# Kernel optimization log

Measured on AMD Instinct MI355X. Metric: run time of the kernel, lower is better.

## Reference

```python
import jax, jax.numpy as jnp
import numpy as np

TAU = 0.5

def setup_inputs() -> dict:
    key = jax.random.key(0)
    kx, ky = jax.random.split(key)
    B, H = 8192, 256
    x = jax.random.normal(kx, (B, H), dtype=jnp.float32)
    y = jax.random.normal(ky, (B, H), dtype=jnp.float32)
    return {"x": x, "y": y}

def reference(x, y):
    # L2-normalize rows
    x_norm = x / jnp.linalg.norm(x, axis=1, keepdims=True)
    y_norm = y / jnp.linalg.norm(y, axis=1, keepdims=True)
    xy_norm = jnp.concatenate([x_norm, y_norm], axis=0)  # [2N, H]
    yx_norm = jnp.concatenate([y_norm, x_norm], axis=0)  # [2N, H]
    # [2N, 2N] cosine-similarity matrix (dominant memory traffic)
    sim_mat_1 = xy_norm @ xy_norm.T
    exp_mat = jnp.exp(sim_mat_1 / TAU)
    exp_row_sum = jnp.sum(exp_mat, axis=1)
    exp_diag = jnp.diagonal(exp_mat)
    denominator = exp_row_sum - exp_diag
    # diag(xy_norm @ yx_norm.T) is the row-wise dot product (avoids redundant NxN matmul)
    pos_sim = jnp.sum(xy_norm * yx_norm, axis=1)
    numerator = jnp.exp(pos_sim / TAU)
    nt_xent = -jnp.log(numerator / denominator)
    return jnp.mean(nt_xent)
```

## Files before the change

### kernel.cpp

```cpp
#include <hip/hip_runtime.h>
#include <hip/hip_bf16.h>
#include <math.h>

constexpr int NROWS = 8192;
constexpr int HDIM  = 256;
constexpr int N2    = 16384;
constexpr int TM    = 256;
constexpr int BK    = 32;
constexpr int NCHUNK = HDIM / BK;
constexpr int PIECE = TM * BK;
constexpr int NTILE = N2 / TM;
constexpr int NBLK  = NTILE * (NTILE + 1) / 2;

constexpr float PRESCALE = 1.69864357f;

typedef __attribute__((ext_vector_type(4))) float floatx4;
typedef __attribute__((ext_vector_type(8))) short shortx8;

__device__ __forceinline__ void async_copy16(const void* gptr, void* lptr) {
    __builtin_amdgcn_global_load_lds(
        (const __attribute__((address_space(1))) unsigned int*)gptr,
        (__attribute__((address_space(3))) unsigned int*)lptr, 16, 0, 0);
}

#define WAIT_VM2()   __builtin_amdgcn_s_waitcnt(0x0F72)
#define WAIT_VM0()   __builtin_amdgcn_s_waitcnt(0x0F70)
#define MEMFENCE()   __asm__ __volatile__("" ::: "memory")
#define RAW_BARRIER() do { MEMFENCE(); __builtin_amdgcn_s_barrier(); MEMFENCE(); } while (0)

#define DPP_ROW_SHL_ADD(v, CTRL) do {                                        \
    union { float f; int i; } _u, _r; _u.f = (v);                            \
    _r.i = __builtin_amdgcn_update_dpp(0, _u.i, (CTRL), 0xF, 0xF, true);     \
    (v) += _r.f; } while (0)

__global__ __launch_bounds__(256) void normalize_kernel(
    const float* __restrict__ x, const float* __restrict__ y,
    __hip_bfloat16* __restrict__ Z, float* __restrict__ pos,
    float* __restrict__ rowsum, float* __restrict__ out)
{
    const int wave = threadIdx.x >> 6, lane = threadIdx.x & 63;
    const int row  = blockIdx.x * 4 + wave;

    const float4 xv = ((const float4*)x)[row * 64 + lane];
    const float4 yv = ((const float4*)y)[row * 64 + lane];

    float sx  = xv.x*xv.x + xv.y*xv.y + xv.z*xv.z + xv.w*xv.w;
    float sy  = yv.x*yv.x + yv.y*yv.y + yv.z*yv.z + yv.w*yv.w;
    float sxy = xv.x*yv.x + xv.y*yv.y + xv.z*yv.z + xv.w*yv.w;
    #pragma unroll
    for (int m = 1; m < 64; m <<= 1) {
        sx  += __shfl_xor(sx,  m);
        sy  += __shfl_xor(sy,  m);
        sxy += __shfl_xor(sxy, m);
    }
    const float rxn = rsqrtf(sx), ryn = rsqrtf(sy);
    const float rx = rxn * PRESCALE, ry = ryn * PRESCALE;

    union { ushort4 u; __hip_bfloat16 h[4]; } zx, zy;
    zx.h[0] = __float2bfloat16(xv.x * rx); zx.h[1] = __float2bfloat16(xv.y * rx);
    zx.h[2] = __float2bfloat16(xv.z * rx); zx.h[3] = __float2bfloat16(xv.w * rx);
    zy.h[0] = __float2bfloat16(yv.x * ry); zy.h[1] = __float2bfloat16(yv.y * ry);
    zy.h[2] = __float2bfloat16(yv.z * ry); zy.h[3] = __float2bfloat16(yv.w * ry);
    ((ushort4*)Z)[row * 64 + lane]             = zx.u;
    ((ushort4*)Z)[(row + NROWS) * 64 + lane]   = zy.u;

    if (lane == 0) {
        const float p = sxy * rxn * ryn;
        pos[row]         = p;
        pos[row + NROWS] = p;
    }
    const int gt = blockIdx.x * 256 + threadIdx.x;
    if (gt < N2) rowsum[gt] = 0.f;
    if (gt == 0) out[0] = 0.f;
}

__global__ __launch_bounds__(1024, 4) void simgemm_kernel(
    const __hip_bfloat16* __restrict__ Z, float* __restrict__ rowsum)
{
    const int b = blockIdx.x;
    const int k = b & 7;
    const int m = b >> 3;
    int bi, bj;
    if (m < 36) {
        int ti = (int)((17.0f - sqrtf(289.0f - 8.0f * (float)m)) * 0.5f);
        if (m < ti * (17 - ti) / 2) ti--;
        else if (m >= (ti + 1) * (16 - ti) / 2) ti++;
        const int tj = ti + (m - ti * (17 - ti) / 2);
        bi = k * 8 + ti;
        bj = k * 8 + tj;
    } else {
        const int m2 = m - 36;
        const int hh = m2 >> 5;
        const int r  = m2 & 31;
        const int h  = hh * 8 + k;
        const int q  = h >> 1;
        const int sub = h & 1;
        int gi = 0;
        #pragma unroll
        for (int t = 6; t > 0; --t)
            if (q >= t * (15 - t) / 2) { gi = t; break; }
        const int gj = gi + 1 + (q - gi * (15 - gi) / 2);
        bi = gi * 8 + sub * 4 + (r >> 3);
        bj = gj * 8 + (r & 7);
    }
    const bool diag = (bi == bj);

    __shared__ alignas(16) __hip_bfloat16 tiles[6 * PIECE];
    __shared__ float rs[TM];
    __shared__ float cs[TM];
    __hip_bfloat16* tA = tiles;
    __hip_bfloat16* tB = tiles + PIECE;

    const int tid  = threadIdx.x;
    const int wave = tid >> 6;
    const int lane = tid & 63;
    const int wm   = wave & 3;
    const int wn   = wave >> 2;
    const int g    = lane >> 4;
    const int m15  = lane & 15;

    if (tid < TM) { rs[tid] = 0.f; cs[tid] = 0.f; }

    const int st_r0  = wave * 16 + (lane >> 2);
    const int st_c   = (lane & 3) ^ ((lane >> 3) & 3);
    const __hip_bfloat16* gA0 = Z + (size_t)(bi * TM + st_r0) * HDIM + st_c * 8;
    const __hip_bfloat16* gB0 = Z + (size_t)(bj * TM + st_r0) * HDIM + st_c * 8;
    __hip_bfloat16* lA0 = tA + (wave * 16) * BK;
    __hip_bfloat16* lB0 = tB + (wave * 16) * BK;

    const int sw = g ^ ((m15 >> 1) & 3);
    const __hip_bfloat16* rA = tA + (wm * 64 + m15) * BK + sw * 8;
    const __hip_bfloat16* rB = tB + (wn * 64 + m15) * BK + sw * 8;

    floatx4 acc[4][4] = {};

    #define STAGE(ck)  do {                                                  \
        const int _o = ((ck) % 3) * 2 * PIECE;                               \
        async_copy16(gA0 + (ck) * BK, lA0 + _o);                             \
        async_copy16(gB0 + (ck) * BK, lB0 + _o);                             \
    } while (0)

    STAGE(0);

    #pragma unroll
    for (int s = 0; s < NCHUNK; ++s) {
        if (s + 1 < NCHUNK) { STAGE(s + 1); WAIT_VM2(); }
        else                { WAIT_VM0(); }
        RAW_BARRIER();

        const int bo = (s % 3) * 2 * PIECE;
        shortx8 af[4], bfr[4];
        #pragma unroll
        for (int f = 0; f < 4; ++f) {
            af[f]  = *(const shortx8*)(rA + bo + f * 16 * BK);
            bfr[f] = *(const shortx8*)(rB + bo + f * 16 * BK);
        }
        __builtin_amdgcn_s_setprio(1);
        #pragma unroll
        for (int fm = 0; fm < 4; ++fm)
            #pragma unroll
            for (int fn = 0; fn < 4; ++fn)
                acc[fm][fn] = __builtin_amdgcn_mfma_f32_16x16x32_bf16(
                    af[fm], bfr[fn], acc[fm][fn], 0, 0, 0);
        __builtin_amdgcn_s_setprio(0);
    }
    #undef STAGE

    float rp[4][4] = {{0.f}};
    float cp[4]    = {0.f};

    if (!diag) {
        #pragma unroll
        for (int fm = 0; fm < 4; ++fm)
            #pragma unroll
            for (int fn = 0; fn < 4; ++fn) {
                const floatx4 a = acc[fm][fn];
                #pragma unroll
                for (int q = 0; q < 4; ++q) {
                    const float e = __builtin_amdgcn_exp2f(a[q]);
                    rp[fm][q] += e;
                    cp[fn]    += e;
                }
            }
    } else {
        #pragma unroll
        for (int fm = 0; fm < 4; ++fm)
            #pragma unroll
            for (int fn = 0; fn < 4; ++fn) {
                const floatx4 a = acc[fm][fn];
                const int cl = wn * 64 + fn * 16 + m15;
                #pragma unroll
                for (int q = 0; q < 4; ++q) {
                    const int rl = wm * 64 + fm * 16 + g * 4 + q;
                    float e = __builtin_amdgcn_exp2f(a[q]);
                    if (cl <= rl) e = 0.f;
                    rp[fm][q] += e;
                    cp[fn]    += e;
                }
            }
    }

    #pragma unroll
    for (int fm = 0; fm < 4; ++fm)
        #pragma unroll
        for (int q = 0; q < 4; ++q) {
            float v = rp[fm][q];
            DPP_ROW_SHL_ADD(v, 0x101);
            DPP_ROW_SHL_ADD(v, 0x102);
            DPP_ROW_SHL_ADD(v, 0x104);
            DPP_ROW_SHL_ADD(v, 0x108);
            rp[fm][q] = v;
        }
    if (m15 == 0) {
        #pragma unroll
        for (int fm = 0; fm < 4; ++fm)
            #pragma unroll
            for (int q = 0; q < 4; ++q)
                atomicAdd(&rs[wm * 64 + fm * 16 + g * 4 + q], rp[fm][q]);
    }

    #pragma unroll
    for (int mask = 16; mask < 64; mask <<= 1)
        #pragma unroll
        for (int fn = 0; fn < 4; ++fn)
            cp[fn] += __shfl_xor(cp[fn], mask);
    if (g == 0) {
        #pragma unroll
        for (int fn = 0; fn < 4; ++fn)
            atomicAdd(&cs[wn * 64 + fn * 16 + m15], cp[fn]);
    }

    __syncthreads();
    if (tid < TM) {
        atomicAdd(&rowsum[(size_t)bi * TM + tid], rs[tid]);
        atomicAdd(&rowsum[(size_t)bj * TM + tid], cs[tid]);
    }
}

__global__ __launch_bounds__(1024) void finalize_kernel(
    const float* __restrict__ rowsum, const float* __restrict__ pos,
    float* __restrict__ out)
{
    const int i = threadIdx.x + blockIdx.x * 1024;
    float s = logf(rowsum[i]) - 2.0f * pos[i];
    #pragma unroll
    for (int off = 32; off; off >>= 1) s += __shfl_down(s, off);
    __shared__ float sh[16];
    const int lt = threadIdx.x;
    if ((lt & 63) == 0) sh[lt >> 6] = s;
    __syncthreads();
    if (lt == 0) {
        float tot = 0.f;
        #pragma unroll
        for (int w = 0; w < 16; ++w) tot += sh[w];
        atomicAdd(out, tot / (float)N2);
    }
}

extern "C" void kernel_launch(void* const* d_in, const int* in_sizes, int n_in,
                              void* d_out, int out_size, void* d_ws, size_t ws_size,
                              hipStream_t stream)
{
    const float* x = (const float*)d_in[0];
    const float* y = (const float*)d_in[1];

    __hip_bfloat16* Z = (__hip_bfloat16*)d_ws;
    float* rowsum = (float*)((char*)d_ws + (size_t)N2 * HDIM * sizeof(__hip_bfloat16));
    float* pos    = rowsum + N2;

    normalize_kernel<<<NROWS / 4, 256, 0, stream>>>(x, y, Z, pos, rowsum, (float*)d_out);
    simgemm_kernel<<<NBLK, 1024, 0, stream>>>(Z, rowsum);
    finalize_kernel<<<N2 / 1024, 1024, 0, stream>>>(rowsum, pos, (float*)d_out);
}
```

Measured before the change: 151.6 us.

## Quantize normalized embeddings to FP8 e4m3 and use FP8 MFMA for similarity GEMM

Normalized rows are now encoded as FP8 e4m3 with a software converter instead of bf16. The similarity GEMM uses fp8 16x16x32 MFMA, with 64-byte K-chunks staged into LDS and a new swizzled fragment layout. This halves operand bytes and LDS traffic and uses the higher-throughput FP8 matrix path. The cost is lower precision in the exponentiated similarities, which may hurt accuracy, plus a costlier scalar conversion in the normalize kernel.

```diff
diff --git a/kernel.cpp b/kernel.cpp
--- a/kernel.cpp
+++ b/kernel.cpp
@@ -6,16 +6,15 @@
 constexpr int HDIM  = 256;
 constexpr int N2    = 16384;
 constexpr int TM    = 256;
-constexpr int BK    = 32;
-constexpr int NCHUNK = HDIM / BK;
-constexpr int PIECE = TM * BK;
+constexpr int BKB   = 64;
+constexpr int NCHUNK = HDIM / BKB;
+constexpr int PIECEB = TM * BKB;
 constexpr int NTILE = N2 / TM;
 constexpr int NBLK  = NTILE * (NTILE + 1) / 2;
 
 constexpr float PRESCALE = 1.69864357f;
 
 typedef __attribute__((ext_vector_type(4))) float floatx4;
-typedef __attribute__((ext_vector_type(8))) short shortx8;
 
 __device__ __forceinline__ void async_copy16(const void* gptr, void* lptr) {
     __builtin_amdgcn_global_load_lds(
@@ -33,9 +32,25 @@
     _r.i = __builtin_amdgcn_update_dpp(0, _u.i, (CTRL), 0xF, 0xF, true);     \
     (v) += _r.f; } while (0)
 
+__device__ __forceinline__ unsigned int f32_to_e4m3(float f) {
+    const float a = fabsf(f);
+    const unsigned int s = f < 0.f ? 0x80u : 0u;
+    if (a < 0.015625f) {
+        int mm = (int)rintf(a * 512.0f);
+        if (mm == 8) return s | 0x08u;
+        return s | (unsigned int)mm;
+    }
+    int e; const float fr = frexpf(a, &e);
+    int mm = (int)rintf(fr * 16.0f) - 8;
+    int E  = e + 6;
+    if (mm == 8) { mm = 0; E += 1; }
+    if (E > 15) { E = 15; mm = 6; }
+    return s | (unsigned int)((E << 3) | mm);
+}
+
 __global__ __launch_bounds__(256) void normalize_kernel(
     const float* __restrict__ x, const float* __restrict__ y,
-    __hip_bfloat16* __restrict__ Z, float* __restrict__ pos,
+    unsigned char* __restrict__ Zb, float* __restrict__ pos,
     float* __restrict__ rowsum, float* __restrict__ out)
 {
     const int wave = threadIdx.x >> 6, lane = threadIdx.x & 63;
@@ -56,13 +71,15 @@
     const float rxn = rsqrtf(sx), ryn = rsqrtf(sy);
     const float rx = rxn * PRESCALE, ry = ryn * PRESCALE;
 
-    union { ushort4 u; __hip_bfloat16 h[4]; } zx, zy;
-    zx.h[0] = __float2bfloat16(xv.x * rx); zx.h[1] = __float2bfloat16(xv.y * rx);
-    zx.h[2] = __float2bfloat16(xv.z * rx); zx.h[3] = __float2bfloat16(xv.w * rx);
-    zy.h[0] = __float2bfloat16(yv.x * ry); zy.h[1] = __float2bfloat16(yv.y * ry);
-    zy.h[2] = __float2bfloat16(yv.z * ry); zy.h[3] = __float2bfloat16(yv.w * ry);
-    ((ushort4*)Z)[row * 64 + lane]             = zx.u;
-    ((ushort4*)Z)[(row + NROWS) * 64 + lane]   = zy.u;
+    const unsigned int px =
+        f32_to_e4m3(xv.x * rx)        | (f32_to_e4m3(xv.y * rx) << 8) |
+        (f32_to_e4m3(xv.z * rx) << 16) | (f32_to_e4m3(xv.w * rx) << 24);
+    const unsigned int py =
+        f32_to_e4m3(yv.x * ry)        | (f32_to_e4m3(yv.y * ry) << 8) |
+        (f32_to_e4m3(yv.z * ry) << 16) | (f32_to_e4m3(yv.w * ry) << 24);
+
+    ((unsigned int*)Zb)[row * 64 + lane]             = px;
+    ((unsigned int*)Zb)[(row + NROWS) * 64 + lane]   = py;
 
     if (lane == 0) {
         const float p = sxy * rxn * ryn;
@@ -75,7 +92,7 @@
 }
 
 __global__ __launch_bounds__(1024, 4) void simgemm_kernel(
-    const __hip_bfloat16* __restrict__ Z, float* __restrict__ rowsum)
+    const unsigned char* __restrict__ Zb, float* __restrict__ rowsum)
 {
     const int b = blockIdx.x;
     const int k = b & 7;
@@ -105,11 +122,9 @@
     }
     const bool diag = (bi == bj);
 
-    __shared__ alignas(16) __hip_bfloat16 tiles[6 * PIECE];
+    __shared__ alignas(16) char tiles[6 * PIECEB];
     __shared__ float rs[TM];
     __shared__ float cs[TM];
-    __hip_bfloat16* tA = tiles;
-    __hip_bfloat16* tB = tiles + PIECE;
 
     const int tid  = threadIdx.x;
     const int wave = tid >> 6;
@@ -121,23 +136,26 @@
 
     if (tid < TM) { rs[tid] = 0.f; cs[tid] = 0.f; }
 
-    const int st_r0  = wave * 16 + (lane >> 2);
-    const int st_c   = (lane & 3) ^ ((lane >> 3) & 3);
-    const __hip_bfloat16* gA0 = Z + (size_t)(bi * TM + st_r0) * HDIM + st_c * 8;
-    const __hip_bfloat16* gB0 = Z + (size_t)(bj * TM + st_r0) * HDIM + st_c * 8;
-    __hip_bfloat16* lA0 = tA + (wave * 16) * BK;
-    __hip_bfloat16* lB0 = tB + (wave * 16) * BK;
-
-    const int sw = g ^ ((m15 >> 1) & 3);
-    const __hip_bfloat16* rA = tA + (wm * 64 + m15) * BK + sw * 8;
-    const __hip_bfloat16* rB = tB + (wn * 64 + m15) * BK + sw * 8;
+    const int st_r0 = wave * 16 + (lane >> 2);
+    const int st_c  = (lane & 3) ^ ((lane >> 3) & 3);
+    const unsigned char* gA0 = Zb + (size_t)(bi * TM + st_r0) * HDIM + st_c * 16;
+    const unsigned char* gB0 = Zb + (size_t)(bj * TM + st_r0) * HDIM + st_c * 16;
+
+    const int xr = (m15 >> 1) & 3;
+    const int s0 = g >> 1;
+    const int ha = (g & 1) * 8;
+    const int off0 = ((s0 ^ xr) * 16) + ha;
+    const int off1 = (((2 + s0) ^ xr) * 16) + ha;
+    const int rowA = (wm * 64 + m15) * BKB;
+    const int rowB = (wn * 64 + m15) * BKB;
 
     floatx4 acc[4][4] = {};
 
     #define STAGE(ck)  do {                                                  \
-        const int _o = ((ck) % 3) * 2 * PIECE;                               \
-        async_copy16(gA0 + (ck) * BK, lA0 + _o);                             \
-        async_copy16(gB0 + (ck) * BK, lB0 + _o);                             \
+        const int _o = ((ck) % 3) * 2 * PIECEB;                              \
+        async_copy16(gA0 + (ck) * BKB, tiles + _o + (wave * 16) * BKB);      \
+        async_copy16(gB0 + (ck) * BKB,                                       \
+                     tiles + _o + PIECEB + (wave * 16) * BKB);               \
     } while (0)
 
     STAGE(0);
@@ -148,20 +166,27 @@
         else                { WAIT_VM0(); }
         RAW_BARRIER();
 
-        const int bo = (s % 3) * 2 * PIECE;
-        shortx8 af[4], bfr[4];
-        #pragma unroll
-        for (int f = 0; f < 4; ++f) {
-            af[f]  = *(const shortx8*)(rA + bo + f * 16 * BK);
-            bfr[f] = *(const shortx8*)(rB + bo + f * 16 * BK);
+        const char* bA = tiles + (s % 3) * 2 * PIECEB;
+        const char* bB = bA + PIECEB;
+        long af[2][4], bfr[2][4];
+        #pragma unroll
+        for (int ks = 0; ks < 2; ++ks) {
+            const int off = ks ? off1 : off0;
+            #pragma unroll
+            for (int f = 0; f < 4; ++f) {
+                af[ks][f]  = *(const long*)(bA + rowA + f * 16 * BKB + off);
+                bfr[ks][f] = *(const long*)(bB + rowB + f * 16 * BKB + off);
+            }
         }
         __builtin_amdgcn_s_setprio(1);
         #pragma unroll
-        for (int fm = 0; fm < 4; ++fm)
-            #pragma unroll
-            for (int fn = 0; fn < 4; ++fn)
-                acc[fm][fn] = __builtin_amdgcn_mfma_f32_16x16x32_bf16(
-                    af[fm], bfr[fn], acc[fm][fn], 0, 0, 0);
+        for (int ks = 0; ks < 2; ++ks)
+            #pragma unroll
+            for (int fm = 0; fm < 4; ++fm)
+                #pragma unroll
+                for (int fn = 0; fn < 4; ++fn)
+                    acc[fm][fn] = __builtin_amdgcn_mfma_f32_16x16x32_fp8_fp8(
+                        af[ks][fm], bfr[ks][fn], acc[fm][fn], 0, 0, 0);
         __builtin_amdgcn_s_setprio(0);
     }
     #undef STAGE
@@ -264,11 +289,11 @@
     const float* x = (const float*)d_in[0];
     const float* y = (const float*)d_in[1];
 
-    __hip_bfloat16* Z = (__hip_bfloat16*)d_ws;
-    float* rowsum = (float*)((char*)d_ws + (size_t)N2 * HDIM * sizeof(__hip_bfloat16));
+    unsigned char* Zb = (unsigned char*)d_ws;
+    float* rowsum = (float*)((char*)d_ws + (size_t)N2 * HDIM);
     float* pos    = rowsum + N2;
 
-    normalize_kernel<<<NROWS / 4, 256, 0, stream>>>(x, y, Z, pos, rowsum, (float*)d_out);
-    simgemm_kernel<<<NBLK, 1024, 0, stream>>>(Z, rowsum);
+    normalize_kernel<<<NROWS / 4, 256, 0, stream>>>(x, y, Zb, pos, rowsum, (float*)d_out);
+    simgemm_kernel<<<NBLK, 1024, 0, stream>>>(Zb, rowsum);
     finalize_kernel<<<N2 / 1024, 1024, 0, stream>>>(rowsum, pos, (float*)d_out);
 }
```

Measured after the change: 153.3 us. Within noise of the previous version (+1.1%).
